# Kernel optimization log

Measured on AMD Instinct MI355X. Metric: run time of the kernel, lower is better.

The kernel has to match this reference:

```python
import jax, jax.numpy as jnp
import numpy as np

N_NODES = 50000

def gcn_conv(x, W, b, src, dst, n):
    # PyG GCNConv: h = x @ W; add self-loops; sym-normalized mean aggregation; + bias
    h = x @ W  # [N, out]
    deg = jax.ops.segment_sum(jnp.ones(src.shape[0], x.dtype), dst, num_segments=n) + 1.0  # +1 self-loop
    dinv = jax.lax.rsqrt(deg)  # deg^{-1/2}
    norm = dinv[src] * dinv[dst]  # [E]
    msg = h[src] * norm[:, None]  # [E, out]
    agg = jax.ops.segment_sum(msg, dst, num_segments=n)
    agg = agg + h * (dinv * dinv)[:, None]  # self-loop contribution, norm = 1/deg
    return agg + b


def setup_inputs() -> dict:
    key = jax.random.key(0)
    ks = jax.random.split(key, 12)
    f1, h1, h2, a = 128, 128, 64, N_NODES
    def glorot(k, shape):
        lim = float(np.sqrt(6.0 / (shape[0] + shape[1])))
        return jax.random.uniform(k, shape, jnp.float32, -lim, lim)
    x = jax.random.normal(ks[0], (N_NODES, f1), jnp.float32)
    edge_index = jax.random.randint(ks[1], (2, 800000), 0, N_NODES, dtype=jnp.int64)
    W1 = glorot(ks[2], (f1, h1)); b1 = jnp.zeros((h1,), jnp.float32)
    W2 = glorot(ks[3], (h1, h2)); b2 = jnp.zeros((h2,), jnp.float32)
    W3 = glorot(ks[4], (h2, 1));  b3 = jnp.zeros((1,), jnp.float32)
    lim4 = float(1.0 / np.sqrt(a))
    W4 = jax.random.uniform(ks[5], (a,), jnp.float32, -lim4, lim4)
    b4 = jax.random.uniform(ks[6], (1,), jnp.float32, -lim4, lim4)
    return {"x": x, "edge_index": edge_index, "W1": W1, "b1": b1,
            "W2": W2, "b2": b2, "W3": W3, "b3": b3, "W4": W4, "b4": b4}


def reference(x, edge_index, W1, b1, W2, b2, W3, b3, W4, b4):
    src, dst = edge_index[0], edge_index[1]
    n = x.shape[0]
    h = jnp.tanh(gcn_conv(x, W1, b1, src, dst, n))
    h = jnp.tanh(gcn_conv(h, W2, b2, src, dst, n))
    h = jnp.tanh(gcn_conv(h, W3, b3, src, dst, n))
    h = h.reshape(-1)  # [N] == action_dim
    out = jnp.dot(W4, h) + b4  # Linear(action_dim, 1) -> [1]
    return out
```

## Files before the change

kernel.cpp:

```cpp
#include <hip/hip_runtime.h>
#include <math.h>


constexpr int BLOCK = 256;
constexpr int SLOTS = 64;
constexpr int DEGS = 32;

template<int K, int M>
__global__ void __launch_bounds__(256) gemm1_fill(const float* __restrict__ X,
                                                  const float* __restrict__ W,
                                                  float* __restrict__ H, int N, int ngemm,
                                                  const int* __restrict__ src,
                                                  const int* __restrict__ dst,
                                                  int* __restrict__ degp,
                                                  unsigned short* __restrict__ slots,
                                                  int E, int nfill) {
    __shared__ float xs[64][64];
    const int rem = blockIdx.x % 3;
    if (rem != 0) {
        int blk = (blockIdx.x / 3) * 2 + (rem - 1);
        if (blk >= nfill) return;
        int base = (blk * blockDim.x + threadIdx.x) * 2;
        if (base + 2 <= E) {
            int2 da = *reinterpret_cast<const int2*>(dst + base);
            int2 sa = *reinterpret_cast<const int2*>(src + base);
            int p0 = atomicAdd(&degp[(size_t)da.x * DEGS], 1);
            int p1 = atomicAdd(&degp[(size_t)da.y * DEGS], 1);
            if (p0 < SLOTS) slots[(size_t)da.x * SLOTS + p0] = (unsigned short)sa.x;
            if (p1 < SLOTS) slots[(size_t)da.y * SLOTS + p1] = (unsigned short)sa.y;
        } else {
            for (int e = base; e < E; ++e) {
                int d = dst[e];
                int p = atomicAdd(&degp[(size_t)d * DEGS], 1);
                if (p < SLOTS) slots[(size_t)d * SLOTS + p] = (unsigned short)src[e];
            }
        }
        return;
    }
    constexpr int BM = 64;
    constexpr int TN = 4;
    constexpr int TX = M / TN;
    constexpr int TY = 256 / TX;
    constexpr int TM = BM / TY;
    constexpr int KH4 = 16;

    int gblk = blockIdx.x / 3;
    if (gblk >= ngemm) return;
    const int tid = threadIdx.x;
    const int n0 = gblk * BM;

    const int tx = tid % TX;
    const int ty = tid / TX;
    const int col0 = tx * TN;
    const int row0 = ty * TM;

    float acc[TM][TN];
#pragma unroll
    for (int r = 0; r < TM; ++r)
#pragma unroll
        for (int c = 0; c < TN; ++c) acc[r][c] = 0.0f;

    const float4* X4 = reinterpret_cast<const float4*>(X);
    const float4* W4 = reinterpret_cast<const float4*>(W);
    constexpr int X4_PER_ROW = K / 4;
    constexpr int W4_PER_ROW = M / 4;

#pragma unroll
    for (int ph = 0; ph < 2; ++ph) {
#pragma unroll
        for (int i = 0; i < 4; ++i) {
            int idx = tid + i * 256;
            int row = idx >> 4;
            int k4 = idx & 15;
            float4 v = make_float4(0.f, 0.f, 0.f, 0.f);
            if (n0 + row < N) v = X4[(size_t)(n0 + row) * X4_PER_ROW + ph * KH4 + k4];
            *reinterpret_cast<float4*>(&xs[row][k4 * 4]) = v;
        }
        __syncthreads();
#pragma unroll 4
        for (int k4 = 0; k4 < KH4; ++k4) {
            int k4g = ph * KH4 + k4;
            float4 wv[4];
#pragma unroll
            for (int i = 0; i < 4; ++i)
                wv[i] = W4[(size_t)(k4g * 4 + i) * W4_PER_ROW + tx];
            float4 xv[TM];
#pragma unroll
            for (int r = 0; r < TM; ++r)
                xv[r] = *reinterpret_cast<const float4*>(&xs[row0 + r][k4 * 4]);
#pragma unroll
            for (int r = 0; r < TM; ++r) {
#pragma unroll
                for (int c = 0; c < TN; ++c) {
                    acc[r][c] = fmaf(xv[r].x, ((float*)&wv[0])[c], acc[r][c]);
                    acc[r][c] = fmaf(xv[r].y, ((float*)&wv[1])[c], acc[r][c]);
                    acc[r][c] = fmaf(xv[r].z, ((float*)&wv[2])[c], acc[r][c]);
                    acc[r][c] = fmaf(xv[r].w, ((float*)&wv[3])[c], acc[r][c]);
                }
            }
        }
        __syncthreads();
    }

#pragma unroll
    for (int r = 0; r < TM; ++r) {
        int row = n0 + row0 + r;
        if (row < N) {
            float4 o;
            o.x = acc[r][0]; o.y = acc[r][1];
            o.z = acc[r][2]; o.w = acc[r][3];
            *reinterpret_cast<float4*>(&H[(size_t)row * M + col0]) = o;
        }
    }
}

__global__ void dinv_scale(const int* __restrict__ degp, int* __restrict__ cnt,
                           float* __restrict__ dinv, float4* __restrict__ H4, int N) {
    int idx = blockIdx.x * blockDim.x + threadIdx.x;
    int n = idx >> 5, q = idx & 31;
    if (n > N) return;
    if (n == N) { if (q == 0) dinv[N] = 0.0f; return; }
    int dg = degp[(size_t)n * DEGS];
    float di = 1.0f / sqrtf((float)dg + 1.0f);
    if (q == 0) { dinv[n] = di; cnt[n] = min(dg, SLOTS); }
    float4 v = H4[idx];
    v.x *= di; v.y *= di; v.z *= di; v.w *= di;
    H4[idx] = v;
}

template<int K, int M>
__global__ void __launch_bounds__(256) gemm_tiled(const float* __restrict__ X,
                                                  const float* __restrict__ W,
                                                  const float* __restrict__ dinv,
                                                  float* __restrict__ H, int N) {
    constexpr int BM = 64;
    constexpr int TN = 4;
    constexpr int TX = M / TN;
    constexpr int TY = 256 / TX;
    constexpr int TM = BM / TY;
    constexpr int K4 = K / 4;

    __shared__ float xs[BM][K];

    const int tid = threadIdx.x;
    const int n0 = blockIdx.x * BM;

    {
        const float4* X4 = reinterpret_cast<const float4*>(X);
        constexpr int F4_PER_ROW = K / 4;
        constexpr int TOT = BM * F4_PER_ROW;
#pragma unroll
        for (int i = 0; i < TOT / 256; ++i) {
            int idx = tid + i * 256;
            int row = idx / F4_PER_ROW;
            int k4 = idx % F4_PER_ROW;
            float4 v = make_float4(0.f, 0.f, 0.f, 0.f);
            if (n0 + row < N) v = X4[(size_t)(n0 + row) * F4_PER_ROW + k4];
            *reinterpret_cast<float4*>(&xs[row][k4 * 4]) = v;
        }
    }
    __syncthreads();

    const int tx = tid % TX;
    const int ty = tid / TX;
    const int col0 = tx * TN;
    const int row0 = ty * TM;

    float acc[TM][TN];
#pragma unroll
    for (int r = 0; r < TM; ++r)
#pragma unroll
        for (int c = 0; c < TN; ++c) acc[r][c] = 0.0f;

    const float4* W4 = reinterpret_cast<const float4*>(W);
    constexpr int W4_PER_ROW = M / 4;

#pragma unroll 4
    for (int k4 = 0; k4 < K4; ++k4) {
        float4 wv[4];
#pragma unroll
        for (int i = 0; i < 4; ++i)
            wv[i] = W4[(size_t)(k4 * 4 + i) * W4_PER_ROW + tx];
        float4 xv[TM];
#pragma unroll
        for (int r = 0; r < TM; ++r)
            xv[r] = *reinterpret_cast<const float4*>(&xs[row0 + r][k4 * 4]);
#pragma unroll
        for (int r = 0; r < TM; ++r) {
#pragma unroll
            for (int c = 0; c < TN; ++c) {
                acc[r][c] = fmaf(xv[r].x, ((float*)&wv[0])[c], acc[r][c]);
                acc[r][c] = fmaf(xv[r].y, ((float*)&wv[1])[c], acc[r][c]);
                acc[r][c] = fmaf(xv[r].z, ((float*)&wv[2])[c], acc[r][c]);
                acc[r][c] = fmaf(xv[r].w, ((float*)&wv[3])[c], acc[r][c]);
            }
        }
    }

#pragma unroll
    for (int r = 0; r < TM; ++r) {
        int row = n0 + row0 + r;
        if (row < N) {
            float di = dinv[row];
            float4 o;
            o.x = acc[r][0] * di; o.y = acc[r][1] * di;
            o.z = acc[r][2] * di; o.w = acc[r][3] * di;
            *reinterpret_cast<float4*>(&H[(size_t)row * M + col0]) = o;
        }
    }
}

__global__ void __launch_bounds__(256) agg128(const int* __restrict__ cntA,
                                              const unsigned short* __restrict__ slots,
                                              const float* __restrict__ dinv,
                                              const float* __restrict__ Hs,
                                              const float* __restrict__ bias,
                                              float* __restrict__ A, int N) {
    int wid = threadIdx.x >> 6;
    int lane = threadIdx.x & 63;
    int n = blockIdx.x * 4 + wid;
    if (n >= N) return;
    int half = lane >> 5, sub = lane & 31;
    const float4* H4 = reinterpret_cast<const float4*>(Hs);
    float4 acc = make_float4(0.f, 0.f, 0.f, 0.f);
    if (half == 0) acc = H4[(size_t)n * 32 + sub];
    int cnt = cntA[n];
    int idxv = (lane < cnt) ? (int)slots[(size_t)n * SLOTS + lane] : N;
    int cnt16 = (cnt + 15) & ~15;
    for (int j = 0; j < cnt16; j += 16) {
        int s0 = __shfl(idxv, j + half);
        int s1 = __shfl(idxv, j + 2 + half);
        int s2 = __shfl(idxv, j + 4 + half);
        int s3 = __shfl(idxv, j + 6 + half);
        int s4 = __shfl(idxv, j + 8 + half);
        int s5 = __shfl(idxv, j + 10 + half);
        int s6 = __shfl(idxv, j + 12 + half);
        int s7 = __shfl(idxv, j + 14 + half);
        float4 v0 = H4[(size_t)s0 * 32 + sub];
        float4 v1 = H4[(size_t)s1 * 32 + sub];
        float4 v2 = H4[(size_t)s2 * 32 + sub];
        float4 v3 = H4[(size_t)s3 * 32 + sub];
        float4 v4 = H4[(size_t)s4 * 32 + sub];
        float4 v5 = H4[(size_t)s5 * 32 + sub];
        float4 v6 = H4[(size_t)s6 * 32 + sub];
        float4 v7 = H4[(size_t)s7 * 32 + sub];
        acc.x += (v0.x + v1.x) + (v2.x + v3.x) + (v4.x + v5.x) + (v6.x + v7.x);
        acc.y += (v0.y + v1.y) + (v2.y + v3.y) + (v4.y + v5.y) + (v6.y + v7.y);
        acc.z += (v0.z + v1.z) + (v2.z + v3.z) + (v4.z + v5.z) + (v6.z + v7.z);
        acc.w += (v0.w + v1.w) + (v2.w + v3.w) + (v4.w + v5.w) + (v6.w + v7.w);
    }
    acc.x += __shfl_down(acc.x, 32);
    acc.y += __shfl_down(acc.y, 32);
    acc.z += __shfl_down(acc.z, 32);
    acc.w += __shfl_down(acc.w, 32);
    if (half == 0) {
        float di = dinv[n];
        float4 b = reinterpret_cast<const float4*>(bias)[sub];
        float4 o;
        o.x = tanhf(acc.x * di + b.x);
        o.y = tanhf(acc.y * di + b.y);
        o.z = tanhf(acc.z * di + b.z);
        o.w = tanhf(acc.w * di + b.w);
        reinterpret_cast<float4*>(A)[(size_t)n * 32 + sub] = o;
    }
}

__global__ void __launch_bounds__(256) agg64_dot3(const int* __restrict__ cntA,
                                                  const unsigned short* __restrict__ slots,
                                                  const float* __restrict__ dinv,
                                                  const float* __restrict__ Hs,
                                                  const float* __restrict__ b2,
                                                  const float* __restrict__ W3,
                                                  float* __restrict__ Hs3, int N) {
    int wid = threadIdx.x >> 6;
    int lane = threadIdx.x & 63;
    int n = blockIdx.x * 4 + wid;
    if (n >= N) return;
    int grp = lane >> 4, sub = lane & 15;
    const float4* H4 = reinterpret_cast<const float4*>(Hs);
    float4 acc = make_float4(0.f, 0.f, 0.f, 0.f);
    if (grp == 0) acc = H4[(size_t)n * 16 + sub];
    int cnt = cntA[n];
    int idxv = (lane < cnt) ? (int)slots[(size_t)n * SLOTS + lane] : N;
    int cnt16 = (cnt + 15) & ~15;
    int j = 0;
    for (; j + 32 <= cnt16; j += 32) {
        int s0 = __shfl(idxv, j + grp);
        int s1 = __shfl(idxv, j + 4 + grp);
        int s2 = __shfl(idxv, j + 8 + grp);
        int s3 = __shfl(idxv, j + 12 + grp);
        int s4 = __shfl(idxv, j + 16 + grp);
        int s5 = __shfl(idxv, j + 20 + grp);
        int s6 = __shfl(idxv, j + 24 + grp);
        int s7 = __shfl(idxv, j + 28 + grp);
        float4 v0 = H4[(size_t)s0 * 16 + sub];
        float4 v1 = H4[(size_t)s1 * 16 + sub];
        float4 v2 = H4[(size_t)s2 * 16 + sub];
        float4 v3 = H4[(size_t)s3 * 16 + sub];
        float4 v4 = H4[(size_t)s4 * 16 + sub];
        float4 v5 = H4[(size_t)s5 * 16 + sub];
        float4 v6 = H4[(size_t)s6 * 16 + sub];
        float4 v7 = H4[(size_t)s7 * 16 + sub];
        acc.x += (v0.x + v1.x) + (v2.x + v3.x) + (v4.x + v5.x) + (v6.x + v7.x);
        acc.y += (v0.y + v1.y) + (v2.y + v3.y) + (v4.y + v5.y) + (v6.y + v7.y);
        acc.z += (v0.z + v1.z) + (v2.z + v3.z) + (v4.z + v5.z) + (v6.z + v7.z);
        acc.w += (v0.w + v1.w) + (v2.w + v3.w) + (v4.w + v5.w) + (v6.w + v7.w);
    }
    for (; j < cnt16; j += 16) {
        int s0 = __shfl(idxv, j + grp);
        int s1 = __shfl(idxv, j + 4 + grp);
        int s2 = __shfl(idxv, j + 8 + grp);
        int s3 = __shfl(idxv, j + 12 + grp);
        float4 v0 = H4[(size_t)s0 * 16 + sub];
        float4 v1 = H4[(size_t)s1 * 16 + sub];
        float4 v2 = H4[(size_t)s2 * 16 + sub];
        float4 v3 = H4[(size_t)s3 * 16 + sub];
        acc.x += (v0.x + v1.x) + (v2.x + v3.x);
        acc.y += (v0.y + v1.y) + (v2.y + v3.y);
        acc.z += (v0.z + v1.z) + (v2.z + v3.z);
        acc.w += (v0.w + v1.w) + (v2.w + v3.w);
    }
    acc.x += __shfl_xor(acc.x, 16);
    acc.y += __shfl_xor(acc.y, 16);
    acc.z += __shfl_xor(acc.z, 16);
    acc.w += __shfl_xor(acc.w, 16);
    acc.x += __shfl_xor(acc.x, 32);
    acc.y += __shfl_xor(acc.y, 32);
    acc.z += __shfl_xor(acc.z, 32);
    acc.w += __shfl_xor(acc.w, 32);
    float di = dinv[n];
    float4 b = reinterpret_cast<const float4*>(b2)[sub];
    float4 w = reinterpret_cast<const float4*>(W3)[sub];
    float t = tanhf(acc.x * di + b.x) * w.x
            + tanhf(acc.y * di + b.y) * w.y
            + tanhf(acc.z * di + b.z) * w.z
            + tanhf(acc.w * di + b.w) * w.w;
#pragma unroll
    for (int off = 1; off < 16; off <<= 1) t += __shfl_xor(t, off);
    if (lane == 0) Hs3[n] = t * di;
}

__global__ void __launch_bounds__(256) agg_dot(const int* __restrict__ cntA,
                                               const unsigned short* __restrict__ slots,
                                               const float* __restrict__ dinv,
                                               const float* __restrict__ Hs,
                                               const float* __restrict__ b3,
                                               const float* __restrict__ W4,
                                               float* __restrict__ partials, int N) {
    __shared__ float sm[4];
    int wid = threadIdx.x >> 6;
    int lane = threadIdx.x & 63;
    int n = blockIdx.x * 4 + wid;
    float p = 0.0f;
    if (n < N) {
        int cnt = cntA[n];
        float acc = (lane < cnt) ? Hs[(int)slots[(size_t)n * SLOTS + lane]] : 0.0f;
#pragma unroll
        for (int off = 32; off > 0; off >>= 1) acc += __shfl_down(acc, off);
        if (lane == 0) {
            float h = tanhf((acc + Hs[n]) * dinv[n] + b3[0]);
            p = W4[n] * h;
        }
    }
    if (lane == 0) sm[wid] = p;
    __syncthreads();
    if (threadIdx.x == 0) partials[blockIdx.x] = sm[0] + sm[1] + sm[2] + sm[3];
}

__global__ void final_sum(const float* __restrict__ partials, int B,
                          const float* __restrict__ b4, float* __restrict__ out) {
    float acc = 0.0f;
    for (int i = threadIdx.x; i < B; i += blockDim.x) acc += partials[i];
#pragma unroll
    for (int off = 32; off > 0; off >>= 1) acc += __shfl_down(acc, off);
    __shared__ float sm[4];
    int lane = threadIdx.x & 63, wid = threadIdx.x >> 6;
    if (lane == 0) sm[wid] = acc;
    __syncthreads();
    if (threadIdx.x == 0) out[0] = sm[0] + sm[1] + sm[2] + sm[3] + b4[0];
}

extern "C" void kernel_launch(void* const* d_in, const int* in_sizes, int n_in,
                              void* d_out, int out_size, void* d_ws, size_t ws_size,
                              hipStream_t stream) {
    const float* x  = (const float*)d_in[0];
    const int*   ei = (const int*)d_in[1];
    const float* W1 = (const float*)d_in[2];
    const float* b1 = (const float*)d_in[3];
    const float* W2 = (const float*)d_in[4];
    const float* b2 = (const float*)d_in[5];
    const float* W3 = (const float*)d_in[6];
    const float* b3 = (const float*)d_in[7];
    const float* W4 = (const float*)d_in[8];
    const float* b4 = (const float*)d_in[9];

    const int N = in_sizes[0] / 128;
    const int E = in_sizes[1] / 2;
    const int* src = ei;
    const int* dst = ei + E;

    const int nblkW = (N + 3) / 4;

    float* base = (float*)d_ws;
    size_t off = 0;
    auto alloc = [&](size_t cnt, size_t align_f) -> float* {
        off = (off + align_f - 1) / align_f * align_f;
        float* p = base + off;
        off += cnt;
        return p;
    };
    int* cnt     = (int*)alloc(N, 1);
    float* dinv  = alloc(N + 1, 1);
    unsigned short* slots = (unsigned short*)alloc((size_t)N * SLOTS / 2, 64);
    float* bufA  = alloc((size_t)(N + 1) * 128, 64);
    float* bufB  = alloc((size_t)N * 128, 64);
    float* partials = alloc(nblkW, 64);

    float* hs2 = bufA;
    int* degp = (int*)bufB;

    const int ngemm = (N + 63) / 64;
    const int nfill = (E + 511) / 512;
    const int fhalf = (nfill + 1) / 2;
    const int nfused = 3 * ((ngemm > fhalf) ? ngemm : fhalf);
    const int nscale = (N * 32 + 32 + BLOCK - 1) / BLOCK;

    hipMemsetAsync(degp, 0, (size_t)N * DEGS * sizeof(int), stream);
    hipMemsetAsync(bufA + (size_t)N * 128, 0, 128 * sizeof(float), stream);
    gemm1_fill<128, 128><<<nfused, 256, 0, stream>>>(x, W1, bufA, N, ngemm,
                                                     src, dst, degp, slots, E, nfill);
    dinv_scale<<<nscale, BLOCK, 0, stream>>>(degp, cnt, dinv, (float4*)bufA, N);

    agg128<<<nblkW, 256, 0, stream>>>(cnt, slots, dinv, bufA, b1, bufB, N);

    gemm_tiled<128, 64><<<ngemm, 256, 0, stream>>>(bufB, W2, dinv, hs2, N);
    hipMemsetAsync(hs2 + (size_t)N * 64, 0, 64 * sizeof(float), stream);
    agg64_dot3<<<nblkW, 256, 0, stream>>>(cnt, slots, dinv, hs2, b2, W3, bufB, N);

    agg_dot<<<nblkW, 256, 0, stream>>>(cnt, slots, dinv, bufB, b3, W4, partials, N);
    final_sum<<<1, BLOCK, 0, stream>>>(partials, nblkW, b4, (float*)d_out);
}
```

Baseline: 288.1 us.

## Split fused GEMM/edge-fill kernel into separate launches with compact degree array

Separates the combined layer-1 GEMM and edge-slot fill kernel into two independent kernels, launched back to back on the stream. It also drops the padded degree layout (one counter per 128-byte stride) in favour of a dense int array. This removes the interleaved block scheduling and shrinks the degree memset. In exchange, the GEMM and the atomic fill no longer overlap, and dense counters may suffer more atomic contention across neighbouring nodes.

```diff
diff --git a/kernel.cpp b/kernel.cpp
--- a/kernel.cpp
+++ b/kernel.cpp
@@ -4,39 +4,25 @@
 
 constexpr int BLOCK = 256;
 constexpr int SLOTS = 64;
-constexpr int DEGS = 32;
+
+__global__ void __launch_bounds__(256) fill(const int* __restrict__ src,
+                                            const int* __restrict__ dst,
+                                            int* __restrict__ deg,
+                                            unsigned short* __restrict__ slots,
+                                            int E) {
+    int e = blockIdx.x * blockDim.x + threadIdx.x;
+    if (e >= E) return;
+    int d = dst[e];
+    int s = src[e];
+    int p = atomicAdd(&deg[d], 1);
+    if (p < SLOTS) slots[(size_t)d * SLOTS + p] = (unsigned short)s;
+}
 
 template<int K, int M>
-__global__ void __launch_bounds__(256) gemm1_fill(const float* __restrict__ X,
-                                                  const float* __restrict__ W,
-                                                  float* __restrict__ H, int N, int ngemm,
-                                                  const int* __restrict__ src,
-                                                  const int* __restrict__ dst,
-                                                  int* __restrict__ degp,
-                                                  unsigned short* __restrict__ slots,
-                                                  int E, int nfill) {
+__global__ void __launch_bounds__(256) gemm1(const float* __restrict__ X,
+                                             const float* __restrict__ W,
+                                             float* __restrict__ H, int N) {
     __shared__ float xs[64][64];
-    const int rem = blockIdx.x % 3;
-    if (rem != 0) {
-        int blk = (blockIdx.x / 3) * 2 + (rem - 1);
-        if (blk >= nfill) return;
-        int base = (blk * blockDim.x + threadIdx.x) * 2;
-        if (base + 2 <= E) {
-            int2 da = *reinterpret_cast<const int2*>(dst + base);
-            int2 sa = *reinterpret_cast<const int2*>(src + base);
-            int p0 = atomicAdd(&degp[(size_t)da.x * DEGS], 1);
-            int p1 = atomicAdd(&degp[(size_t)da.y * DEGS], 1);
-            if (p0 < SLOTS) slots[(size_t)da.x * SLOTS + p0] = (unsigned short)sa.x;
-            if (p1 < SLOTS) slots[(size_t)da.y * SLOTS + p1] = (unsigned short)sa.y;
-        } else {
-            for (int e = base; e < E; ++e) {
-                int d = dst[e];
-                int p = atomicAdd(&degp[(size_t)d * DEGS], 1);
-                if (p < SLOTS) slots[(size_t)d * SLOTS + p] = (unsigned short)src[e];
-            }
-        }
-        return;
-    }
     constexpr int BM = 64;
     constexpr int TN = 4;
     constexpr int TX = M / TN;
@@ -44,10 +30,8 @@
     constexpr int TM = BM / TY;
     constexpr int KH4 = 16;
 
-    int gblk = blockIdx.x / 3;
-    if (gblk >= ngemm) return;
     const int tid = threadIdx.x;
-    const int n0 = gblk * BM;
+    const int n0 = blockIdx.x * BM;
 
     const int tx = tid % TX;
     const int ty = tid / TX;
@@ -114,13 +98,13 @@
     }
 }
 
-__global__ void dinv_scale(const int* __restrict__ degp, int* __restrict__ cnt,
+__global__ void dinv_scale(const int* __restrict__ deg, int* __restrict__ cnt,
                            float* __restrict__ dinv, float4* __restrict__ H4, int N) {
     int idx = blockIdx.x * blockDim.x + threadIdx.x;
     int n = idx >> 5, q = idx & 31;
     if (n > N) return;
     if (n == N) { if (q == 0) dinv[N] = 0.0f; return; }
-    int dg = degp[(size_t)n * DEGS];
+    int dg = deg[n];
     float di = 1.0f / sqrtf((float)dg + 1.0f);
     if (q == 0) { dinv[n] = di; cnt[n] = min(dg, SLOTS); }
     float4 v = H4[idx];
@@ -409,6 +393,7 @@
         off += cnt;
         return p;
     };
+    int* deg     = (int*)alloc(N, 1);
     int* cnt     = (int*)alloc(N, 1);
     float* dinv  = alloc(N + 1, 1);
     unsigned short* slots = (unsigned short*)alloc((size_t)N * SLOTS / 2, 64);
@@ -417,19 +402,18 @@
     float* partials = alloc(nblkW, 64);
 
     float* hs2 = bufA;
-    int* degp = (int*)bufB;
 
     const int ngemm = (N + 63) / 64;
-    const int nfill = (E + 511) / 512;
-    const int fhalf = (nfill + 1) / 2;
-    const int nfused = 3 * ((ngemm > fhalf) ? ngemm : fhalf);
+    const int nfillb = (E + BLOCK - 1) / BLOCK;
     const int nscale = (N * 32 + 32 + BLOCK - 1) / BLOCK;
 
-    hipMemsetAsync(degp, 0, (size_t)N * DEGS * sizeof(int), stream);
+    hipMemsetAsync(deg, 0, (size_t)N * sizeof(int), stream);
     hipMemsetAsync(bufA + (size_t)N * 128, 0, 128 * sizeof(float), stream);
-    gemm1_fill<128, 128><<<nfused, 256, 0, stream>>>(x, W1, bufA, N, ngemm,
-                                                     src, dst, degp, slots, E, nfill);
-    dinv_scale<<<nscale, BLOCK, 0, stream>>>(degp, cnt, dinv, (float4*)bufA, N);
+    fill<<<nfillb, BLOCK, 0, stream>>>(src, dst, deg, slots, E);
+
+    gemm1<128, 128><<<ngemm, 256, 0, stream>>>(x, W1, bufA, N);
+
+    dinv_scale<<<nscale, BLOCK, 0, stream>>>(deg, cnt, dinv, (float4*)bufA, N);
 
     agg128<<<nblkW, 256, 0, stream>>>(cnt, slots, dinv, bufA, b1, bufB, N);
 
```

Result: slower. 308.0 us (+6.9%).

## Store GEMM outputs in fp16 to halve gather traffic in aggregation

Applied to the files above, without the earlier changes.

The layer-1 and layer-2 transformed features are now written as packed half2 values, and the aggregation kernels unpack them to fp32 for accumulation. This halves the bytes moved by the random neighbor gathers that dominate the aggregation kernels. The degree counters also move from padded per-node slots (one per 32 ints) to a dense array, which shrinks the memset but puts more atomics on shared cache lines. The cost is reduced precision in the stored features.

```diff
diff --git a/kernel.cpp b/kernel.cpp
--- a/kernel.cpp
+++ b/kernel.cpp
@@ -1,18 +1,27 @@
 #include <hip/hip_runtime.h>
+#include <hip/hip_fp16.h>
 #include <math.h>
 
 
 constexpr int BLOCK = 256;
 constexpr int SLOTS = 64;
-constexpr int DEGS = 32;
+
+__device__ inline unsigned int pack_h2(float a, float b) {
+    __half2 h = __floats2half2_rn(a, b);
+    return *reinterpret_cast<unsigned int*>(&h);
+}
+__device__ inline float2 unpack_h2(unsigned int u) {
+    __half2 h = *reinterpret_cast<__half2*>(&u);
+    return __half22float2(h);
+}
 
 template<int K, int M>
 __global__ void __launch_bounds__(256) gemm1_fill(const float* __restrict__ X,
                                                   const float* __restrict__ W,
-                                                  float* __restrict__ H, int N, int ngemm,
+                                                  __half* __restrict__ H, int N, int ngemm,
                                                   const int* __restrict__ src,
                                                   const int* __restrict__ dst,
-                                                  int* __restrict__ degp,
+                                                  int* __restrict__ deg,
                                                   unsigned short* __restrict__ slots,
                                                   int E, int nfill) {
     __shared__ float xs[64][64];
@@ -24,14 +33,14 @@
         if (base + 2 <= E) {
             int2 da = *reinterpret_cast<const int2*>(dst + base);
             int2 sa = *reinterpret_cast<const int2*>(src + base);
-            int p0 = atomicAdd(&degp[(size_t)da.x * DEGS], 1);
-            int p1 = atomicAdd(&degp[(size_t)da.y * DEGS], 1);
+            int p0 = atomicAdd(&deg[da.x], 1);
+            int p1 = atomicAdd(&deg[da.y], 1);
             if (p0 < SLOTS) slots[(size_t)da.x * SLOTS + p0] = (unsigned short)sa.x;
             if (p1 < SLOTS) slots[(size_t)da.y * SLOTS + p1] = (unsigned short)sa.y;
         } else {
             for (int e = base; e < E; ++e) {
                 int d = dst[e];
-                int p = atomicAdd(&degp[(size_t)d * DEGS], 1);
+                int p = atomicAdd(&deg[d], 1);
                 if (p < SLOTS) slots[(size_t)d * SLOTS + p] = (unsigned short)src[e];
             }
         }
@@ -106,33 +115,37 @@
     for (int r = 0; r < TM; ++r) {
         int row = n0 + row0 + r;
         if (row < N) {
-            float4 o;
-            o.x = acc[r][0]; o.y = acc[r][1];
-            o.z = acc[r][2]; o.w = acc[r][3];
-            *reinterpret_cast<float4*>(&H[(size_t)row * M + col0]) = o;
-        }
-    }
-}
-
-__global__ void dinv_scale(const int* __restrict__ degp, int* __restrict__ cnt,
-                           float* __restrict__ dinv, float4* __restrict__ H4, int N) {
+            uint2 o;
+            o.x = pack_h2(acc[r][0], acc[r][1]);
+            o.y = pack_h2(acc[r][2], acc[r][3]);
+            *reinterpret_cast<uint2*>(&H[(size_t)row * M + col0]) = o;
+        }
+    }
+}
+
+__global__ void dinv_scale(const int* __restrict__ deg, int* __restrict__ cnt,
+                           float* __restrict__ dinv, uint2* __restrict__ Hh, int N) {
     int idx = blockIdx.x * blockDim.x + threadIdx.x;
     int n = idx >> 5, q = idx & 31;
     if (n > N) return;
     if (n == N) { if (q == 0) dinv[N] = 0.0f; return; }
-    int dg = degp[(size_t)n * DEGS];
+    int dg = deg[n];
     float di = 1.0f / sqrtf((float)dg + 1.0f);
     if (q == 0) { dinv[n] = di; cnt[n] = min(dg, SLOTS); }
-    float4 v = H4[idx];
-    v.x *= di; v.y *= di; v.z *= di; v.w *= di;
-    H4[idx] = v;
+    uint2 u = Hh[idx];
+    float2 a = unpack_h2(u.x);
+    float2 b = unpack_h2(u.y);
+    uint2 o;
+    o.x = pack_h2(a.x * di, a.y * di);
+    o.y = pack_h2(b.x * di, b.y * di);
+    Hh[idx] = o;
 }
 
 template<int K, int M>
 __global__ void __launch_bounds__(256) gemm_tiled(const float* __restrict__ X,
                                                   const float* __restrict__ W,
                                                   const float* __restrict__ dinv,
-                                                  float* __restrict__ H, int N) {
+                                                  __half* __restrict__ H, int N) {
     constexpr int BM = 64;
     constexpr int TN = 4;
     constexpr int TX = M / TN;
@@ -202,10 +215,10 @@
         int row = n0 + row0 + r;
         if (row < N) {
             float di = dinv[row];
-            float4 o;
-            o.x = acc[r][0] * di; o.y = acc[r][1] * di;
-            o.z = acc[r][2] * di; o.w = acc[r][3] * di;
-            *reinterpret_cast<float4*>(&H[(size_t)row * M + col0]) = o;
+            uint2 o;
+            o.x = pack_h2(acc[r][0] * di, acc[r][1] * di);
+            o.y = pack_h2(acc[r][2] * di, acc[r][3] * di);
+            *reinterpret_cast<uint2*>(&H[(size_t)row * M + col0]) = o;
         }
     }
 }
@@ -213,7 +226,7 @@
 __global__ void __launch_bounds__(256) agg128(const int* __restrict__ cntA,
                                               const unsigned short* __restrict__ slots,
                                               const float* __restrict__ dinv,
-                                              const float* __restrict__ Hs,
+                                              const __half* __restrict__ Hs,
                                               const float* __restrict__ bias,
                                               float* __restrict__ A, int N) {
     int wid = threadIdx.x >> 6;
@@ -221,9 +234,13 @@
     int n = blockIdx.x * 4 + wid;
     if (n >= N) return;
     int half = lane >> 5, sub = lane & 31;
-    const float4* H4 = reinterpret_cast<const float4*>(Hs);
+    const uint2* H2 = reinterpret_cast<const uint2*>(Hs);
     float4 acc = make_float4(0.f, 0.f, 0.f, 0.f);
-    if (half == 0) acc = H4[(size_t)n * 32 + sub];
+    if (half == 0) {
+        uint2 u = H2[(size_t)n * 32 + sub];
+        float2 a = unpack_h2(u.x), b = unpack_h2(u.y);
+        acc.x = a.x; acc.y = a.y; acc.z = b.x; acc.w = b.y;
+    }
     int cnt = cntA[n];
     int idxv = (lane < cnt) ? (int)slots[(size_t)n * SLOTS + lane] : N;
     int cnt16 = (cnt + 15) & ~15;
@@ -236,18 +253,26 @@
         int s5 = __shfl(idxv, j + 10 + half);
         int s6 = __shfl(idxv, j + 12 + half);
         int s7 = __shfl(idxv, j + 14 + half);
-        float4 v0 = H4[(size_t)s0 * 32 + sub];
-        float4 v1 = H4[(size_t)s1 * 32 + sub];
-        float4 v2 = H4[(size_t)s2 * 32 + sub];
-        float4 v3 = H4[(size_t)s3 * 32 + sub];
-        float4 v4 = H4[(size_t)s4 * 32 + sub];
-        float4 v5 = H4[(size_t)s5 * 32 + sub];
-        float4 v6 = H4[(size_t)s6 * 32 + sub];
-        float4 v7 = H4[(size_t)s7 * 32 + sub];
-        acc.x += (v0.x + v1.x) + (v2.x + v3.x) + (v4.x + v5.x) + (v6.x + v7.x);
-        acc.y += (v0.y + v1.y) + (v2.y + v3.y) + (v4.y + v5.y) + (v6.y + v7.y);
-        acc.z += (v0.z + v1.z) + (v2.z + v3.z) + (v4.z + v5.z) + (v6.z + v7.z);
-        acc.w += (v0.w + v1.w) + (v2.w + v3.w) + (v4.w + v5.w) + (v6.w + v7.w);
+        uint2 u0 = H2[(size_t)s0 * 32 + sub];
+        uint2 u1 = H2[(size_t)s1 * 32 + sub];
+        uint2 u2 = H2[(size_t)s2 * 32 + sub];
+        uint2 u3 = H2[(size_t)s3 * 32 + sub];
+        uint2 u4 = H2[(size_t)s4 * 32 + sub];
+        uint2 u5 = H2[(size_t)s5 * 32 + sub];
+        uint2 u6 = H2[(size_t)s6 * 32 + sub];
+        uint2 u7 = H2[(size_t)s7 * 32 + sub];
+        float2 a0 = unpack_h2(u0.x), b0 = unpack_h2(u0.y);
+        float2 a1 = unpack_h2(u1.x), b1 = unpack_h2(u1.y);
+        float2 a2 = unpack_h2(u2.x), b2 = unpack_h2(u2.y);
+        float2 a3 = unpack_h2(u3.x), b3 = unpack_h2(u3.y);
+        float2 a4 = unpack_h2(u4.x), b4 = unpack_h2(u4.y);
+        float2 a5 = unpack_h2(u5.x), b5 = unpack_h2(u5.y);
+        float2 a6 = unpack_h2(u6.x), b6 = unpack_h2(u6.y);
+        float2 a7 = unpack_h2(u7.x), b7 = unpack_h2(u7.y);
+        acc.x += (a0.x + a1.x) + (a2.x + a3.x) + (a4.x + a5.x) + (a6.x + a7.x);
+        acc.y += (a0.y + a1.y) + (a2.y + a3.y) + (a4.y + a5.y) + (a6.y + a7.y);
+        acc.z += (b0.x + b1.x) + (b2.x + b3.x) + (b4.x + b5.x) + (b6.x + b7.x);
+        acc.w += (b0.y + b1.y) + (b2.y + b3.y) + (b4.y + b5.y) + (b6.y + b7.y);
     }
     acc.x += __shfl_down(acc.x, 32);
     acc.y += __shfl_down(acc.y, 32);
@@ -268,7 +293,7 @@
 __global__ void __launch_bounds__(256) agg64_dot3(const int* __restrict__ cntA,
                                                   const unsigned short* __restrict__ slots,
                                                   const float* __restrict__ dinv,
-                                                  const float* __restrict__ Hs,
+                                                  const __half* __restrict__ Hs,
                                                   const float* __restrict__ b2,
                                                   const float* __restrict__ W3,
                                                   float* __restrict__ Hs3, int N) {
@@ -277,9 +302,13 @@
     int n = blockIdx.x * 4 + wid;
     if (n >= N) return;
     int grp = lane >> 4, sub = lane & 15;
-    const float4* H4 = reinterpret_cast<const float4*>(Hs);
+    const uint2* H2 = reinterpret_cast<const uint2*>(Hs);
     float4 acc = make_float4(0.f, 0.f, 0.f, 0.f);
-    if (grp == 0) acc = H4[(size_t)n * 16 + sub];
+    if (grp == 0) {
+        uint2 u = H2[(size_t)n * 16 + sub];
+        float2 a = unpack_h2(u.x), b = unpack_h2(u.y);
+        acc.x = a.x; acc.y = a.y; acc.z = b.x; acc.w = b.y;
+    }
     int cnt = cntA[n];
     int idxv = (lane < cnt) ? (int)slots[(size_t)n * SLOTS + lane] : N;
     int cnt16 = (cnt + 15) & ~15;
@@ -293,32 +322,44 @@
         int s5 = __shfl(idxv, j + 20 + grp);
         int s6 = __shfl(idxv, j + 24 + grp);
         int s7 = __shfl(idxv, j + 28 + grp);
-        float4 v0 = H4[(size_t)s0 * 16 + sub];
-        float4 v1 = H4[(size_t)s1 * 16 + sub];
-        float4 v2 = H4[(size_t)s2 * 16 + sub];
-        float4 v3 = H4[(size_t)s3 * 16 + sub];
-        float4 v4 = H4[(size_t)s4 * 16 + sub];
-        float4 v5 = H4[(size_t)s5 * 16 + sub];
-        float4 v6 = H4[(size_t)s6 * 16 + sub];
-        float4 v7 = H4[(size_t)s7 * 16 + sub];
-        acc.x += (v0.x + v1.x) + (v2.x + v3.x) + (v4.x + v5.x) + (v6.x + v7.x);
-        acc.y += (v0.y + v1.y) + (v2.y + v3.y) + (v4.y + v5.y) + (v6.y + v7.y);
-        acc.z += (v0.z + v1.z) + (v2.z + v3.z) + (v4.z + v5.z) + (v6.z + v7.z);
-        acc.w += (v0.w + v1.w) + (v2.w + v3.w) + (v4.w + v5.w) + (v6.w + v7.w);
+        uint2 u0 = H2[(size_t)s0 * 16 + sub];
+        uint2 u1 = H2[(size_t)s1 * 16 + sub];
+        uint2 u2 = H2[(size_t)s2 * 16 + sub];
+        uint2 u3 = H2[(size_t)s3 * 16 + sub];
+        uint2 u4 = H2[(size_t)s4 * 16 + sub];
+        uint2 u5 = H2[(size_t)s5 * 16 + sub];
+        uint2 u6 = H2[(size_t)s6 * 16 + sub];
+        uint2 u7 = H2[(size_t)s7 * 16 + sub];
+        float2 a0 = unpack_h2(u0.x), b0 = unpack_h2(u0.y);
+        float2 a1 = unpack_h2(u1.x), b1 = unpack_h2(u1.y);
+        float2 a2 = unpack_h2(u2.x), b2f = unpack_h2(u2.y);
+        float2 a3 = unpack_h2(u3.x), b3f = unpack_h2(u3.y);
+        float2 a4 = unpack_h2(u4.x), b4f = unpack_h2(u4.y);
+        float2 a5 = unpack_h2(u5.x), b5f = unpack_h2(u5.y);
+        float2 a6 = unpack_h2(u6.x), b6f = unpack_h2(u6.y);
+        float2 a7 = unpack_h2(u7.x), b7f = unpack_h2(u7.y);
+        acc.x += (a0.x + a1.x) + (a2.x + a3.x) + (a4.x + a5.x) + (a6.x + a7.x);
+        acc.y += (a0.y + a1.y) + (a2.y + a3.y) + (a4.y + a5.y) + (a6.y + a7.y);
+        acc.z += (b0.x + b1.x) + (b2f.x + b3f.x) + (b4f.x + b5f.x) + (b6f.x + b7f.x);
+        acc.w += (b0.y + b1.y) + (b2f.y + b3f.y) + (b4f.y + b5f.y) + (b6f.y + b7f.y);
     }
     for (; j < cnt16; j += 16) {
         int s0 = __shfl(idxv, j + grp);
         int s1 = __shfl(idxv, j + 4 + grp);
         int s2 = __shfl(idxv, j + 8 + grp);
         int s3 = __shfl(idxv, j + 12 + grp);
-        float4 v0 = H4[(size_t)s0 * 16 + sub];
-        float4 v1 = H4[(size_t)s1 * 16 + sub];
-        float4 v2 = H4[(size_t)s2 * 16 + sub];
-        float4 v3 = H4[(size_t)s3 * 16 + sub];
-        acc.x += (v0.x + v1.x) + (v2.x + v3.x);
-        acc.y += (v0.y + v1.y) + (v2.y + v3.y);
-        acc.z += (v0.z + v1.z) + (v2.z + v3.z);
-        acc.w += (v0.w + v1.w) + (v2.w + v3.w);
+        uint2 u0 = H2[(size_t)s0 * 16 + sub];
+        uint2 u1 = H2[(size_t)s1 * 16 + sub];
+        uint2 u2 = H2[(size_t)s2 * 16 + sub];
+        uint2 u3 = H2[(size_t)s3 * 16 + sub];
+        float2 a0 = unpack_h2(u0.x), b0 = unpack_h2(u0.y);
+        float2 a1 = unpack_h2(u1.x), b1 = unpack_h2(u1.y);
+        float2 a2 = unpack_h2(u2.x), b2f = unpack_h2(u2.y);
+        float2 a3 = unpack_h2(u3.x), b3f = unpack_h2(u3.y);
+        acc.x += (a0.x + a1.x) + (a2.x + a3.x);
+        acc.y += (a0.y + a1.y) + (a2.y + a3.y);
+        acc.z += (b0.x + b1.x) + (b2f.x + b3f.x);
+        acc.w += (b0.y + b1.y) + (b2f.y + b3f.y);
     }
     acc.x += __shfl_xor(acc.x, 16);
     acc.y += __shfl_xor(acc.y, 16);
@@ -409,15 +450,15 @@
         off += cnt;
         return p;
     };
+    int* deg     = (int*)alloc(N, 1);
     int* cnt     = (int*)alloc(N, 1);
     float* dinv  = alloc(N + 1, 1);
     unsigned short* slots = (unsigned short*)alloc((size_t)N * SLOTS / 2, 64);
-    float* bufA  = alloc((size_t)(N + 1) * 128, 64);
+    __half* H1h  = (__half*)alloc((size_t)(N + 1) * 64, 64);
     float* bufB  = alloc((size_t)N * 128, 64);
     float* partials = alloc(nblkW, 64);
 
-    float* hs2 = bufA;
-    int* degp = (int*)bufB;
+    __half* hs2 = H1h;
 
     const int ngemm = (N + 63) / 64;
     const int nfill = (E + 511) / 512;
@@ -425,16 +466,16 @@
     const int nfused = 3 * ((ngemm > fhalf) ? ngemm : fhalf);
     const int nscale = (N * 32 + 32 + BLOCK - 1) / BLOCK;
 
-    hipMemsetAsync(degp, 0, (size_t)N * DEGS * sizeof(int), stream);
-    hipMemsetAsync(bufA + (size_t)N * 128, 0, 128 * sizeof(float), stream);
-    gemm1_fill<128, 128><<<nfused, 256, 0, stream>>>(x, W1, bufA, N, ngemm,
-                                                     src, dst, degp, slots, E, nfill);
-    dinv_scale<<<nscale, BLOCK, 0, stream>>>(degp, cnt, dinv, (float4*)bufA, N);
-
-    agg128<<<nblkW, 256, 0, stream>>>(cnt, slots, dinv, bufA, b1, bufB, N);
+    hipMemsetAsync(deg, 0, (size_t)N * sizeof(int), stream);
+    hipMemsetAsync(H1h + (size_t)N * 128, 0, 128 * sizeof(__half), stream);
+    gemm1_fill<128, 128><<<nfused, 256, 0, stream>>>(x, W1, H1h, N, ngemm,
+                                                     src, dst, deg, slots, E, nfill);
+    dinv_scale<<<nscale, BLOCK, 0, stream>>>(deg, cnt, dinv, (uint2*)H1h, N);
+
+    agg128<<<nblkW, 256, 0, stream>>>(cnt, slots, dinv, H1h, b1, bufB, N);
 
     gemm_tiled<128, 64><<<ngemm, 256, 0, stream>>>(bufB, W2, dinv, hs2, N);
-    hipMemsetAsync(hs2 + (size_t)N * 64, 0, 64 * sizeof(float), stream);
+    hipMemsetAsync(hs2 + (size_t)N * 64, 0, 64 * sizeof(__half), stream);
     agg64_dot3<<<nblkW, 256, 0, stream>>>(cnt, slots, dinv, hs2, b2, W3, bufB, N);
 
     agg_dot<<<nblkW, 256, 0, stream>>>(cnt, slots, dinv, bufB, b3, W4, partials, N);
```

Measured after the change: 254.8 us. 11.5% less time.
